# Kernel tuning notes

Measured on AMD Instinct MI355X. Metric: run time of the kernel, lower is better.

The kernel has to match this reference:

```python
import jax, jax.numpy as jnp
import numpy as np

VEC_DIM = 3          # Cl(3,0): 3 positive-signature basis vectors
BASIS_DIM = 1 << VEC_DIM  # 8 basis blades
BATCH, IN_F, OUT_F = 512, 512, 512


def cayley_table(n: int = VEC_DIM) -> np.ndarray:
    """Geometric-product tensor G[i, j, k] for Cl(n,0) with blades as bitmasks.
    e_a * e_b = sign(a,b) * e_{a XOR b}; Euclidean metric so e_i^2 = +1.
    Only 2^(2n) of the 2^(3n) entries are nonzero (highly sparse)."""
    dim = 1 << n
    G = np.zeros((dim, dim, dim), dtype=np.float32)
    for a in range(dim):
        for b in range(dim):
            # sign from counting transpositions to bring blade product to canonical order
            swaps, t = 0, a >> 1
            while t:
                swaps += bin(t & b).count("1")
                t >>= 1
            G[a, b, a ^ b] = -1.0 if (swaps & 1) else 1.0
    return G


def setup_inputs() -> dict:
    key = jax.random.key(0)
    kx, kw, kb = jax.random.split(key, 3)
    x = jax.random.normal(kx, (BATCH, IN_F, BASIS_DIM), dtype=jnp.float32)
    W = jax.random.normal(kw, (IN_F, OUT_F, BASIS_DIM), dtype=jnp.float32)
    b = jax.random.normal(kb, (OUT_F, BASIS_DIM), dtype=jnp.float32)
    G = jnp.asarray(cayley_table())  # exact Cl(3,0) geometric-product tensor
    return {"x": x, "W": W, "b": b, "G": G}


def reference(x, W, b, G):
    # out[b,o,k] = sum_{i,j,p} G[i,j,k] * x[b,p,i] * W[p,o,j]  (+ bias)
    out = jnp.einsum("ijk,bpi,poj->bok", G, x, W)
    return out + b
```

## Files before the change

kernel.cpp:

```cpp
#include <hip/hip_runtime.h>
#include <hip/hip_bf16.h>
#include <stdint.h>

typedef __attribute__((ext_vector_type(8))) short short8;
typedef __attribute__((ext_vector_type(4))) float floatx4;

__device__ __forceinline__ unsigned short bfu(float a) {
    return __builtin_bit_cast(unsigned short, __float2bfloat16(a));
}
__device__ __forceinline__ uint32_t pkbf(float a, float b) {
    return (uint32_t)bfu(a) | ((uint32_t)bfu(b) << 16);
}


__global__ __launch_bounds__(256) void pack_all(
    const float* __restrict__ x, const float* __restrict__ W,
    unsigned short* __restrict__ Abuf, unsigned short* __restrict__ BT)
{
    const int t = threadIdx.x;
    if (blockIdx.x < 512) {
        __shared__ unsigned short TX[4][1024];
        const int b = blockIdx.x;
        const float4* src = (const float4*)(x + ((size_t)b * 512 + 2 * t) * 8);
        float4 f[4] = {src[0], src[1], src[2], src[3]};
        #pragma unroll
        for (int pp = 0; pp < 2; ++pp) {
            const float a0 = f[2*pp].x, a1 = f[2*pp].y, a2 = f[2*pp].z, a3 = f[2*pp].w;
            const float a4 = f[2*pp+1].x, a5 = f[2*pp+1].y, a6 = f[2*pp+1].z, a7 = f[2*pp+1].w;
            const int c = 4 * t + 2 * pp;
            TX[0][c] = bfu(a0 + a4); TX[0][c+1] = bfu(a1 - a5);
            TX[1][c] = bfu(a3 + a7); TX[1][c+1] = bfu(a6 - a2);
            TX[2][c] = bfu(a1 + a5); TX[2][c+1] = bfu(a0 - a4);
            TX[3][c] = bfu(a6 + a2); TX[3][c+1] = bfu(a7 - a3);
        }
        __syncthreads();
        const int tr = t >> 6, off = (t & 63) * 16;
        uint4* dst = (uint4*)(Abuf + (size_t)(2*b + (tr >> 1)) * 2048 + (tr & 1) * 1024 + off);
        const uint4* s4 = (const uint4*)&TX[tr][off];
        dst[0] = s4[0]; dst[1] = s4[1];
    } else {
        const int wb = blockIdx.x - 512;
        const int pbase = (wb & 7) * 64;
        const int o0 = (wb >> 3) * 16;
        const int o = o0 + (t & 15);
        const int pc = t >> 4;
        float R[4][2][2], I[4][2][2];
        #pragma unroll
        for (int u = 0; u < 4; ++u) {
            const float4* src = (const float4*)(W + ((size_t)(pbase + pc * 4 + u) * 512 + o) * 8);
            float4 lo = src[0], hi = src[1];
            R[u][0][0] = lo.x + hi.x;  I[u][0][0] = lo.w + hi.w;
            R[u][0][1] = lo.y - hi.y;  I[u][0][1] = hi.z - lo.z;
            R[u][1][0] = lo.y + hi.y;  I[u][1][0] = hi.z + lo.z;
            R[u][1][1] = lo.x - hi.x;  I[u][1][1] = hi.w - lo.w;
        }
        const int kbase = 2 * pbase + pc * 8;
        #pragma unroll
        for (int part = 0; part < 2; ++part)
            #pragma unroll
            for (int pN = 0; pN < 2; ++pN)
                #pragma unroll
                for (int c = 0; c < 2; ++c) {
                    uint4 v; uint32_t* vv = (uint32_t*)&v;
                    #pragma unroll
                    for (int u = 0; u < 4; ++u) {
                        const float v0 = (part == 0) ? (pN ? I[u][0][c] : R[u][0][c])
                                                     : (pN ? R[u][0][c] : -I[u][0][c]);
                        const float v1 = (part == 0) ? (pN ? I[u][1][c] : R[u][1][c])
                                                     : (pN ? R[u][1][c] : -I[u][1][c]);
                        vv[u] = pkbf(v0, v1);
                    }
                    const int n = 4 * o + 2 * pN + c;
                    *(uint4*)&BT[(size_t)n * 2048 + part * 1024 + kbase] = v;
                }
    }
}

__global__ __launch_bounds__(512) void iso_gemm2(
    const unsigned short* __restrict__ AB,
    const unsigned short* __restrict__ BB,
    const float* __restrict__ bias,
    float*       __restrict__ out)
{
    __shared__ __align__(16) unsigned char smem[98304];
    const int t = threadIdx.x, lane = t & 63, wave = t >> 6;
    const int wn = wave & 1;
    const int g  = wave >> 1;
    const int l15 = lane & 15, q = lane >> 4;

    const int lin = blockIdx.y * 16 + blockIdx.x;
    const int xcd = lin & 7, sx = lin >> 3;
    const int tn = (xcd & 3) * 4 + (sx & 3);
    const int tm = (xcd >> 2) * 8 + (sx >> 2);
    const int m0 = tm * 64, v0 = tn * 128;

    const unsigned short* arow[4];
    const unsigned short* brow[4];
    #pragma unroll
    for (int f = 0; f < 4; ++f) {
        arow[f] = AB + (size_t)(m0 + f * 16 + l15) * 2048;
        brow[f] = BB + (size_t)(v0 + wn * 64 + f * 16 + l15) * 2048;
    }
    const int kbase = g * 512 + q * 8;

    floatx4 acc[4][4] = {};
    short8 abuf[2][4], bbuf[2][4];

    #pragma unroll
    for (int f = 0; f < 4; ++f) {
        abuf[0][f] = *(const short8*)(arow[f] + kbase);
        bbuf[0][f] = *(const short8*)(brow[f] + kbase);
    }
    #pragma unroll 2
    for (int it = 0; it < 16; ++it) {
        const int cb = it & 1, nb = cb ^ 1;
        if (it < 15) {
            const int kk = kbase + (it + 1) * 32;
            #pragma unroll
            for (int f = 0; f < 4; ++f) {
                abuf[nb][f] = *(const short8*)(arow[f] + kk);
                bbuf[nb][f] = *(const short8*)(brow[f] + kk);
            }
        }
        #pragma unroll
        for (int fm = 0; fm < 4; ++fm)
            #pragma unroll
            for (int fn = 0; fn < 4; ++fn)
                acc[fm][fn] = __builtin_amdgcn_mfma_f32_16x16x32_bf16(
                    abuf[cb][fm], bbuf[cb][fn], acc[fm][fn], 0, 0, 0);
    }

    __syncthreads();
    if (g > 0) {
        float* r = (float*)(smem + ((g - 1) * 2 + wn) * 16384);
        #pragma unroll
        for (int f = 0; f < 16; ++f)
            *(floatx4*)&r[f * 256 + lane * 4] = acc[f >> 2][f & 3];
    }
    __syncthreads();
    if (g == 0) {
        #pragma unroll
        for (int gg = 1; gg < 4; ++gg) {
            const float* r = (const float*)(smem + ((gg - 1) * 2 + wn) * 16384);
            #pragma unroll
            for (int f = 0; f < 16; ++f)
                acc[f >> 2][f & 3] += *(const floatx4*)&r[f * 256 + lane * 4];
        }
    }
    __syncthreads();
    float* Cf = (float*)smem;
    if (g == 0) {
        #pragma unroll
        for (int fm = 0; fm < 4; ++fm)
            #pragma unroll
            for (int fn = 0; fn < 4; ++fn)
                #pragma unroll
                for (int rr = 0; rr < 4; ++rr) {
                    const int row = fm * 16 + q * 4 + rr;
                    const int col = wn * 64 + fn * 16 + l15;
                    Cf[row * 130 + col] = acc[fm][fn][rr];
                }
    }
    __syncthreads();
    const int b0 = m0 >> 1, o0 = v0 >> 2;
    #pragma unroll
    for (int rnd = 0; rnd < 2; ++rnd) {
        const int pi = rnd * 512 + t;
        const int o_l = pi & 31, b_l = pi >> 5;
        const float* r0 = &Cf[(2 * b_l) * 130 + 4 * o_l];
        const float* r1 = r0 + 130;
        const float Cr00 = r0[0], Cr01 = r0[1], Ci00 = r0[2], Ci01 = r0[3];
        const float Cr10 = r1[0], Cr11 = r1[1], Ci10 = r1[2], Ci11 = r1[3];
        const float a0 = 0.5f * (Cr00 + Cr11), a7 = 0.5f * (Ci00 + Ci11);
        const float a4 = 0.5f * (Cr00 - Cr11), a3 = 0.5f * (Ci00 - Ci11);
        const float a1 = 0.5f * (Cr01 + Cr10), a6 = 0.5f * (Ci01 + Ci10);
        const float a2 = 0.5f * (Ci10 - Ci01), a5 = 0.5f * (Cr10 - Cr01);
        const int o = o0 + o_l, b = b0 + b_l;
        const float* bp = bias + o * 8;
        float4 lo = {a0 + bp[0], a1 + bp[1], a2 + bp[2], a3 + bp[3]};
        float4 hi = {a4 + bp[4], a5 + bp[5], a6 + bp[6], a7 + bp[7]};
        float* op = out + ((size_t)b * 512 + o) * 8;
        *(float4*)op = lo;
        *(float4*)(op + 4) = hi;
    }
}

__device__ __align__(16) const uint32_t SGN[4][4] = {
    {0x00000000u, 0x80000000u, 0x80000000u, 0x80008000u},
    {0x80000000u, 0x00000000u, 0x00000000u, 0x00008000u},
    {0x80000000u, 0x80008000u, 0x00000000u, 0x80000000u},
    {0x00000000u, 0x00008000u, 0x80000000u, 0x00000000u},
};
__device__ __forceinline__ uint32_t swap16(uint32_t a) { return (a >> 16) | (a << 16); }
__device__ __forceinline__ uint4 xperm2(uint4 v, int kp) {
    const bool s1 = (kp & 1) != 0;
    uint32_t x1 = s1 ? v.y : v.x, y1 = s1 ? v.x : v.y, z1 = s1 ? v.w : v.z, w1 = s1 ? v.z : v.w;
    const bool s2 = (kp & 2) != 0;
    uint4 r; r.x = s2 ? z1 : x1; r.y = s2 ? w1 : y1; r.z = s2 ? x1 : z1; r.w = s2 ? y1 : w1;
    return r;
}
__global__ __launch_bounds__(512) void gp_linear_legacy(
    const float* __restrict__ xg_raw, const float* __restrict__ wg,
    const float* __restrict__ bias, float* __restrict__ out)
{
    __shared__ __align__(16) unsigned short As[128 * 64];
    __shared__ __align__(16) unsigned short Bs[8 * 64 * 8];
    const int t = threadIdx.x, lane = t & 63, wave = t >> 6;
    const int m0 = blockIdx.y * 128, n0 = blockIdx.x * 64;
    const int ap = t & 7, akp = (t >> 3) & 3, ab = t >> 5, ak0 = akp * 2;
    const uint4 mask = *(const uint4*)SGN[akp];
    const int wm = wave & 3, wnn = wave >> 2, l15 = lane & 15, q = lane >> 4;
    floatx4 acc[2][2] = {};
    const float4* xg = (const float4*)xg_raw;
    const int bg0 = m0 >> 3;
    float4 ax0, ax1, bw0, bw1;
    {
        const size_t aidx = ((size_t)(bg0 + ab) * 512 + ap) * 2;
        ax0 = xg[aidx]; ax1 = xg[aidx + 1];
        const float* gsrc = wg + (((size_t)wave * 512 + n0) << 3) + (lane << 3);
        bw0 = *(const float4*)gsrc; bw1 = *(const float4*)(gsrc + 4);
    }
    for (int kt = 0; kt < 64; ++kt) {
        __syncthreads();
        {
            uint4 v;
            v.x = pkbf(ax0.x, ax0.y); v.y = pkbf(ax0.z, ax0.w);
            v.z = pkbf(ax1.x, ax1.y); v.w = pkbf(ax1.z, ax1.w);
            uint4 pk = xperm2(v, akp), r0, p1, r1;
            r0.x = pk.x ^ mask.x; r0.y = pk.y ^ mask.y; r0.z = pk.z ^ mask.z; r0.w = pk.w ^ mask.w;
            p1.x = swap16(pk.x); p1.y = swap16(pk.y); p1.z = swap16(pk.z); p1.w = swap16(pk.w);
            r1.x = p1.x ^ mask.x; r1.y = p1.y ^ mask.y; r1.z = p1.z ^ mask.z; r1.w = p1.w ^ mask.w;
            const int row0 = ab * 8 + ak0;
            *(uint4*)&As[row0 * 64 + ((ap ^ ak0) << 3)] = r0;
            *(uint4*)&As[(row0 + 1) * 64 + ((ap ^ (ak0 + 1)) << 3)] = r1;
        }
        {
            uint4 b0;
            b0.x = pkbf(bw0.x, bw0.y); b0.y = pkbf(bw0.z, bw0.w);
            b0.z = pkbf(bw1.x, bw1.y); b0.w = pkbf(bw1.z, bw1.w);
            *(uint4*)&Bs[t << 3] = b0;
        }
        __syncthreads();
        if (kt + 1 < 64) {
            const int p0n = (kt + 1) * 8;
            const size_t aidx = ((size_t)(bg0 + ab) * 512 + p0n + ap) * 2;
            ax0 = xg[aidx]; ax1 = xg[aidx + 1];
            const float* gsrc = wg + (((size_t)(p0n + wave) * 512 + n0) << 3) + (lane << 3);
            bw0 = *(const float4*)gsrc; bw1 = *(const float4*)(gsrc + 4);
        }
        #pragma unroll
        for (int ks = 0; ks < 2; ++ks) {
            const int cb = ks * 4 + q;
            short8 a[2], bfr[2];
            #pragma unroll
            for (int fm = 0; fm < 2; ++fm) {
                const int row = wm * 32 + fm * 16 + l15;
                a[fm] = *(const short8*)&As[row * 64 + ((cb ^ (l15 & 7)) << 3)];
            }
            #pragma unroll
            for (int fn = 0; fn < 2; ++fn) {
                const int nl = wnn * 32 + fn * 16 + l15;
                bfr[fn] = *(const short8*)&Bs[((cb * 64) + nl) << 3];
            }
            #pragma unroll
            for (int fm = 0; fm < 2; ++fm)
                #pragma unroll
                for (int fn = 0; fn < 2; ++fn)
                    acc[fm][fn] = __builtin_amdgcn_mfma_f32_16x16x32_bf16(a[fm], bfr[fn], acc[fm][fn], 0, 0, 0);
        }
    }
    #pragma unroll
    for (int fm = 0; fm < 2; ++fm)
        #pragma unroll
        for (int fn = 0; fn < 2; ++fn) {
            const int n = n0 + wnn * 32 + fn * 16 + l15;
            #pragma unroll
            for (int r = 0; r < 4; ++r) {
                const int m = m0 + wm * 32 + fm * 16 + q * 4 + r;
                const int bi = m >> 3, k = m & 7;
                out[(size_t)bi * 4096 + n * 8 + k] = acc[fm][fn][r] + bias[n * 8 + k];
            }
        }
}

extern "C" void kernel_launch(void* const* d_in, const int* in_sizes, int n_in,
                              void* d_out, int out_size, void* d_ws, size_t ws_size,
                              hipStream_t stream) {
    const float* x  = (const float*)d_in[0];
    const float* W  = (const float*)d_in[1];
    const float* bb = (const float*)d_in[2];
    float* out = (float*)d_out;

    const size_t abytes = (size_t)1024 * 2048 * sizeof(unsigned short);
    const size_t bbytes = (size_t)2048 * 2048 * sizeof(unsigned short);
    if (ws_size >= abytes + bbytes) {
        unsigned short* Abuf = (unsigned short*)d_ws;
        unsigned short* Bbuf = (unsigned short*)((char*)d_ws + abytes);
        pack_all<<<768, 256, 0, stream>>>(x, W, Abuf, Bbuf);
        iso_gemm2<<<dim3(16, 16), 512, 0, stream>>>(Abuf, Bbuf, bb, out);
    } else {
        gp_linear_legacy<<<dim3(8, 32), dim3(512), 0, stream>>>(x, W, bb, out);
    }
}
```

Measured before the change: 107.5 us.

## Stage GEMM operands through LDS with async global_load_lds and double buffering

Replaces the direct global-to-register operand loads in the split-K GEMM with asynchronous global_load_lds copies into a swizzled, double-buffered shared-memory tile, read back via ds loads. Tiles shrink to 64x64 with 256-thread blocks (two blocks per CU), and the grid doubles to 512 blocks. The aim is fewer redundant global reads, since A and B fragments are now shared across waves, and better latency hiding. In exchange it adds a barrier per k-step and LDS bank traffic, and each wave now covers a k-slice of a shared tile instead of an independent k range.

```diff
diff --git a/kernel.cpp b/kernel.cpp
--- a/kernel.cpp
+++ b/kernel.cpp
@@ -76,63 +76,78 @@
     }
 }
 
-__global__ __launch_bounds__(512) void iso_gemm2(
+#define GLL(src, dstoff) \
+    __builtin_amdgcn_global_load_lds((const __attribute__((address_space(1))) uint32_t*)(src), \
+        (__attribute__((address_space(3))) uint32_t*)(smem + (dstoff)), 16, 0, 0)
+
+__global__ __launch_bounds__(256, 2) void iso_gemm3(
     const unsigned short* __restrict__ AB,
     const unsigned short* __restrict__ BB,
     const float* __restrict__ bias,
     float*       __restrict__ out)
 {
-    __shared__ __align__(16) unsigned char smem[98304];
+    __shared__ __align__(16) unsigned char smem[65536];
     const int t = threadIdx.x, lane = t & 63, wave = t >> 6;
-    const int wn = wave & 1;
-    const int g  = wave >> 1;
+    const int g = wave;
     const int l15 = lane & 15, q = lane >> 4;
 
-    const int lin = blockIdx.y * 16 + blockIdx.x;
+    const int lin = blockIdx.y * 32 + blockIdx.x;
     const int xcd = lin & 7, sx = lin >> 3;
-    const int tn = (xcd & 3) * 4 + (sx & 3);
-    const int tm = (xcd >> 2) * 8 + (sx >> 2);
-    const int m0 = tm * 64, v0 = tn * 128;
-
-    const unsigned short* arow[4];
-    const unsigned short* brow[4];
+    const int tm = (xcd >> 2) * 8 + (sx & 7);
+    const int tn = (xcd & 3) * 8 + (sx >> 3);
+    const int m0 = tm * 64, v0 = tn * 64;
+
+    const unsigned short* a_srcs[4]; int a_dst[4];
+    const unsigned short* b_srcs[4]; int b_dst[4];
     #pragma unroll
-    for (int f = 0; f < 4; ++f) {
-        arow[f] = AB + (size_t)(m0 + f * 16 + l15) * 2048;
-        brow[f] = BB + (size_t)(v0 + wn * 64 + f * 16 + l15) * 2048;
-    }
-    const int kbase = g * 512 + q * 8;
+    for (int i = 0; i < 4; ++i) {
+        const int sid = (wave * 4 + i) * 64 + lane;
+        const int row = sid >> 4, slot = sid & 15, chunk = slot ^ (row & 7);
+        a_srcs[i] = AB + (size_t)(m0 + row) * 2048 + chunk * 8;
+        a_dst[i] = (wave * 4 + i) * 1024;
+        b_srcs[i] = BB + (size_t)(v0 + row) * 2048 + chunk * 8;
+        b_dst[i] = 16384 + (wave * 4 + i) * 1024;
+    }
+
+    const int slot = (g * 4 + q) ^ (l15 & 7);
+    const int a_off = l15 * 256 + slot * 16;
+    const int b_off = 16384 + l15 * 256 + slot * 16;
 
     floatx4 acc[4][4] = {};
-    short8 abuf[2][4], bbuf[2][4];
 
     #pragma unroll
-    for (int f = 0; f < 4; ++f) {
-        abuf[0][f] = *(const short8*)(arow[f] + kbase);
-        bbuf[0][f] = *(const short8*)(brow[f] + kbase);
-    }
-    #pragma unroll 2
-    for (int it = 0; it < 16; ++it) {
-        const int cb = it & 1, nb = cb ^ 1;
-        if (it < 15) {
-            const int kk = kbase + (it + 1) * 32;
-            #pragma unroll
-            for (int f = 0; f < 4; ++f) {
-                abuf[nb][f] = *(const short8*)(arow[f] + kk);
-                bbuf[nb][f] = *(const short8*)(brow[f] + kk);
+    for (int i = 0; i < 4; ++i) { GLL(a_srcs[i], a_dst[i]); GLL(b_srcs[i], b_dst[i]); }
+
+    for (int kt = 0; kt < 16; ++kt) {
+        __syncthreads();
+        const int cur = (kt & 1) * 32768;
+        if (kt + 1 < 16) {
+            const int nxt = ((kt + 1) & 1) * 32768;
+            const int poff = (kt + 1) * 128;
+            #pragma unroll
+            for (int i = 0; i < 4; ++i) {
+                GLL(a_srcs[i] + poff, nxt + a_dst[i]);
+                GLL(b_srcs[i] + poff, nxt + b_dst[i]);
             }
         }
+        short8 af[4], bf[4];
+        #pragma unroll
+        for (int fm = 0; fm < 4; ++fm)
+            af[fm] = *(const short8*)&smem[cur + a_off + fm * 4096];
+        #pragma unroll
+        for (int fn = 0; fn < 4; ++fn)
+            bf[fn] = *(const short8*)&smem[cur + b_off + fn * 4096];
         #pragma unroll
         for (int fm = 0; fm < 4; ++fm)
             #pragma unroll
             for (int fn = 0; fn < 4; ++fn)
                 acc[fm][fn] = __builtin_amdgcn_mfma_f32_16x16x32_bf16(
-                    abuf[cb][fm], bbuf[cb][fn], acc[fm][fn], 0, 0, 0);
+                    af[fm], bf[fn], acc[fm][fn], 0, 0, 0);
     }
 
     __syncthreads();
     if (g > 0) {
-        float* r = (float*)(smem + ((g - 1) * 2 + wn) * 16384);
+        float* r = (float*)(smem + (g - 1) * 16384);
         #pragma unroll
         for (int f = 0; f < 16; ++f)
             *(floatx4*)&r[f * 256 + lane * 4] = acc[f >> 2][f & 3];
@@ -141,7 +156,7 @@
     if (g == 0) {
         #pragma unroll
         for (int gg = 1; gg < 4; ++gg) {
-            const float* r = (const float*)(smem + ((gg - 1) * 2 + wn) * 16384);
+            const float* r = (const float*)(smem + (gg - 1) * 16384);
             #pragma unroll
             for (int f = 0; f < 16; ++f)
                 acc[f >> 2][f & 3] += *(const floatx4*)&r[f * 256 + lane * 4];
@@ -157,18 +172,18 @@
                 #pragma unroll
                 for (int rr = 0; rr < 4; ++rr) {
                     const int row = fm * 16 + q * 4 + rr;
-                    const int col = wn * 64 + fn * 16 + l15;
-                    Cf[row * 130 + col] = acc[fm][fn][rr];
+                    const int col = fn * 16 + l15;
+                    Cf[row * 66 + col] = acc[fm][fn][rr];
                 }
     }
     __syncthreads();
     const int b0 = m0 >> 1, o0 = v0 >> 2;
     #pragma unroll
     for (int rnd = 0; rnd < 2; ++rnd) {
-        const int pi = rnd * 512 + t;
-        const int o_l = pi & 31, b_l = pi >> 5;
-        const float* r0 = &Cf[(2 * b_l) * 130 + 4 * o_l];
-        const float* r1 = r0 + 130;
+        const int pi = rnd * 256 + t;
+        const int o_l = pi & 15, b_l = pi >> 4;
+        const float* r0 = &Cf[(2 * b_l) * 66 + 4 * o_l];
+        const float* r1 = r0 + 66;
         const float Cr00 = r0[0], Cr01 = r0[1], Ci00 = r0[2], Ci01 = r0[3];
         const float Cr10 = r1[0], Cr11 = r1[1], Ci10 = r1[2], Ci11 = r1[3];
         const float a0 = 0.5f * (Cr00 + Cr11), a7 = 0.5f * (Ci00 + Ci11);
@@ -297,7 +312,7 @@
         unsigned short* Abuf = (unsigned short*)d_ws;
         unsigned short* Bbuf = (unsigned short*)((char*)d_ws + abytes);
         pack_all<<<768, 256, 0, stream>>>(x, W, Abuf, Bbuf);
-        iso_gemm2<<<dim3(16, 16), 512, 0, stream>>>(Abuf, Bbuf, bb, out);
+        iso_gemm3<<<dim3(32, 16), 256, 0, stream>>>(Abuf, Bbuf, bb, out);
     } else {
         gp_linear_legacy<<<dim3(8, 32), dim3(512), 0, stream>>>(x, W, bb, out);
     }
```

New measurement: 89.62 us. 1.2x faster.
